# Kernel optimization log

Hardware: AMD Instinct MI355X
Metric: run time of the kernel (lower is better)

## Reference

```python
import jax, jax.numpy as jnp
import numpy as np

B = 4          # documents per batch
L = 128        # unique candidate entity links
S = 2048       # predicted spans (max over batch)
N = 1 + L + S  # root + links + spans


def setup_inputs() -> dict:
    key = jax.random.key(0)
    k1, k2, k3 = jax.random.split(key, 3)
    # coref/linking edge scores over [root | links | spans] x [root | links | spans]
    scores = jax.random.normal(k1, (B, N, N), dtype=jnp.float32) * 0.1
    eye = jnp.eye(N, dtype=jnp.float32)
    # z mask: all admissible edges -- no self loops, no incoming edges to root
    z_mask = jnp.ones((B, N, N), dtype=jnp.float32) * (1.0 - eye)[None]
    z_mask = z_mask.at[:, :, 0].set(0.0)
    # target mask: sparse subset of z edges + root->all so a spanning
    # arborescence always exists (mirrors the gold cluster / gold link edges)
    tgt = (jax.random.uniform(k2, (B, N, N)) < 0.05).astype(jnp.float32) * z_mask
    tgt = tgt.at[:, 0, 1:].set(1.0)
    # ragged valid lengths per batch element (1 + unique_links_len + n_pred_spans)
    lengths = jnp.array([N, N - 256, N - 512, N - 64], dtype=jnp.int32)
    return {"scores": scores, "target_mask": tgt, "z_mask": z_mask, "lengths": lengths}


def _mtt_log_partition(scores, mask, lengths):
    """Matrix-tree theorem log-partition: logdet of the root-minor of the
    Laplacian of exp(scores) restricted to edges in `mask` and to the first
    `lengths[b]` nodes of each batch element."""
    n = scores.shape[-1]
    valid = (jnp.arange(n)[None, :] < lengths[:, None]).astype(scores.dtype)  # [B,N]
    w = jnp.exp(scores) * mask * valid[:, :, None] * valid[:, None, :]        # [B,N,N]
    colsum = jnp.sum(w, axis=-2)                                              # incoming weight per node
    lap = colsum[:, :, None] * jnp.eye(n, dtype=scores.dtype)[None] - w       # L = D_in - W
    minor = lap[:, 1:, 1:]                                                    # drop root row/col
    # pad the diagonal of invalid (past-length) nodes with 1 so they
    # contribute logdet 0 instead of making the minor singular
    pad = 1.0 - valid[:, 1:]
    minor = minor + pad[:, :, None] * jnp.eye(n - 1, dtype=scores.dtype)[None]
    _, logdet = jnp.linalg.slogdet(minor)
    return logdet


def reference(scores, target_mask, z_mask, lengths):
    log_z = _mtt_log_partition(scores, z_mask, lengths)        # log partition over all arborescences
    log_t = _mtt_log_partition(scores, target_mask, lengths)   # log weight of gold arborescences
    return jnp.mean(log_z - log_t)                             # MTT negative log-likelihood
```

## Files before the change

### kernel.cpp

```cpp
#include <hip/hip_runtime.h>
#include <math.h>

#define NFULL 2177
#define NN    2176
#define NMAT  8
#define NBATCH 4
#define LDST  68
#define ATILES 68
#define FRAGM ((size_t)ATILES * 8 * 512)

typedef unsigned int  u32;
typedef unsigned short u16;
typedef __attribute__((ext_vector_type(8)))  short short8;
typedef __attribute__((ext_vector_type(16))) float f32x16;

__device__ inline void bf16split(float x, u16& hi, u16& lo) {
  u32 xb = __float_as_uint(x);
  u32 h = (xb + 0x7FFFu + ((xb >> 16) & 1u)) >> 16;
  float r = x - __uint_as_float(h << 16);
  u32 rb = __float_as_uint(r);
  u32 l = (rb + 0x7FFFu + ((rb >> 16) & 1u)) >> 16;
  hi = (u16)h; lo = (u16)l;
}

__device__ inline void packstore(short* P, size_t off, const u16 v[8]) {
  *(uint4*)(P + off) = make_uint4(v[0] | ((u32)v[1] << 16), v[2] | ((u32)v[3] << 16),
                                  v[4] | ((u32)v[5] << 16), v[6] | ((u32)v[7] << 16));
}

__device__ inline void frag_from_lds(const float* X, int locbase, int kl, int l,
                                     short* Phi, short* Plo, size_t off) {
  const float* p = &X[(locbase + (l & 31)) * LDST + kl];
  float4 v0 = *(const float4*)&p[0];
  float4 v1 = *(const float4*)&p[4];
  u16 hi[8], lo[8];
  bf16split(v0.x, hi[0], lo[0]); bf16split(v0.y, hi[1], lo[1]);
  bf16split(v0.z, hi[2], lo[2]); bf16split(v0.w, hi[3], lo[3]);
  bf16split(v1.x, hi[4], lo[4]); bf16split(v1.y, hi[5], lo[5]);
  bf16split(v1.z, hi[6], lo[6]); bf16split(v1.w, hi[7], lo[7]);
  packstore(Phi, off, hi);
  packstore(Plo, off, lo);
}

__device__ inline void load64(float* X, const float* A, int r0, int c0, int tid) {
#pragma unroll
  for (int it = 0; it < 4; ++it) {
    int f = tid + it * 256;
    int r = f >> 4, c4 = f & 15;
    *(float4*)&X[r * LDST + c4 * 4] = *(const float4*)&A[(size_t)(r0 + r) * NN + c0 + c4 * 4];
  }
}
__device__ inline void store64(const float* X, float* A, int r0, int c0, int tid) {
#pragma unroll
  for (int it = 0; it < 4; ++it) {
    int f = tid + it * 256;
    int r = f >> 4, c4 = f & 15;
    *(float4*)&A[(size_t)(r0 + r) * NN + c0 + c4 * 4] = *(const float4*)&X[r * LDST + c4 * 4];
  }
}

__device__ inline void factor64(float* D, int tid) {
  for (int j = 0; j < 63; ++j) {
    float inv = 1.0f / D[j * LDST + j];
    for (int r = j + 1 + tid; r < 64; r += 256) D[r * LDST + j] *= inv;
    __syncthreads();
    int cc = j + 1 + (tid & 63);
    for (int rr = j + 1 + (tid >> 6); rr < 64; rr += 4)
      if (cc < 64) D[rr * LDST + cc] -= D[rr * LDST + j] * D[j * LDST + cc];
    __syncthreads();
  }
}

__device__ inline void inv_upper64(const float* S, float* V, float* scr, int tid) {
  if (tid < 64) {
    int o = (tid >> 5) * 32, j = tid & 31;
    V[(o + j) * LDST + o + j] = 1.0f / S[(o + j) * LDST + o + j];
    for (int i = j - 1; i >= 0; --i) {
      float a = 0.f;
      for (int t = i + 1; t <= j; ++t) a += S[(o + i) * LDST + o + t] * V[(o + t) * LDST + o + j];
      V[(o + i) * LDST + o + j] = -a / S[(o + i) * LDST + o + i];
    }
    for (int i = j + 1; i < 32; ++i) V[(o + i) * LDST + o + j] = 0.f;
  }
  for (int e = tid; e < 1024; e += 256) V[(32 + (e >> 5)) * LDST + (e & 31)] = 0.f;
  __syncthreads();
  for (int e = tid; e < 1024; e += 256) {
    int a = e >> 5, c = e & 31; float s = 0.f;
    for (int t = 0; t < 32; ++t) s += S[a * LDST + 32 + t] * V[(32 + t) * LDST + 32 + c];
    scr[a * 33 + c] = s;
  }
  __syncthreads();
  for (int e = tid; e < 1024; e += 256) {
    int a = e >> 5, c = e & 31; float s = 0.f;
    for (int t = 0; t < 32; ++t) s += V[a * LDST + t] * scr[t * 33 + c];
    V[a * LDST + 32 + c] = -s;
  }
  __syncthreads();
}

__device__ inline void inv_lower64(const float* S, float* V, float* scr, int tid) {
  if (tid < 64) {
    int o = (tid >> 5) * 32, j = tid & 31;
    V[(o + j) * LDST + o + j] = 1.0f;
    for (int i = j + 1; i < 32; ++i) {
      float a = 0.f;
      for (int t = j; t < i; ++t) a += S[(o + i) * LDST + o + t] * V[(o + t) * LDST + o + j];
      V[(o + i) * LDST + o + j] = -a;
    }
    for (int i = 0; i < j; ++i) V[(o + i) * LDST + o + j] = 0.f;
  }
  for (int e = tid; e < 1024; e += 256) V[(e >> 5) * LDST + 32 + (e & 31)] = 0.f;
  __syncthreads();
  for (int e = tid; e < 1024; e += 256) {
    int a = e >> 5, c = e & 31; float s = 0.f;
    for (int t = 0; t < 32; ++t) s += S[(32 + a) * LDST + t] * V[t * LDST + c];
    scr[a * 33 + c] = s;
  }
  __syncthreads();
  for (int e = tid; e < 1024; e += 256) {
    int a = e >> 5, c = e & 31; float s = 0.f;
    for (int t = 0; t < 32; ++t) s += V[(32 + a) * LDST + 32 + t] * scr[t * 33 + c];
    V[(32 + a) * LDST + c] = -s;
  }
  __syncthreads();
}

__device__ inline void gemm64(const float* P, const float* Q, float acc[4][4], int r0, int c0) {
#pragma unroll
  for (int i = 0; i < 4; ++i)
#pragma unroll
    for (int j = 0; j < 4; ++j) acc[i][j] = 0.f;
  for (int kk = 0; kk < 64; kk += 4) {
    float4 p[4], q[4];
#pragma unroll
    for (int i = 0; i < 4; ++i) p[i] = *(const float4*)&P[(r0 + i) * LDST + kk];
#pragma unroll
    for (int t = 0; t < 4; ++t) q[t] = *(const float4*)&Q[(kk + t) * LDST + c0];
#pragma unroll
    for (int t = 0; t < 4; ++t) {
      float4 qt = q[t];
#pragma unroll
      for (int i = 0; i < 4; ++i) {
        float pv = ((const float*)&p[i])[t];
        acc[i][0] += pv * qt.x; acc[i][1] += pv * qt.y;
        acc[i][2] += pv * qt.z; acc[i][3] += pv * qt.w;
      }
    }
  }
}

__device__ inline void gemm64_bt(const float* P, const float* Q, float acc[4][4], int r0, int c0) {
#pragma unroll
  for (int i = 0; i < 4; ++i)
#pragma unroll
    for (int j = 0; j < 4; ++j) acc[i][j] = 0.f;
  for (int kk = 0; kk < 64; kk += 4) {
    float4 p[4], q[4];
#pragma unroll
    for (int i = 0; i < 4; ++i) p[i] = *(const float4*)&P[(r0 + i) * LDST + kk];
#pragma unroll
    for (int j = 0; j < 4; ++j) q[j] = *(const float4*)&Q[(c0 + j) * LDST + kk];
#pragma unroll
    for (int t = 0; t < 4; ++t)
#pragma unroll
      for (int i = 0; i < 4; ++i) {
        float pv = ((const float*)&p[i])[t];
#pragma unroll
        for (int j = 0; j < 4; ++j) acc[i][j] += pv * ((const float*)&q[j])[t];
      }
  }
}

__device__ inline void rmw_tile(float* __restrict__ A, int R0, int C0, const f32x16& ac) {
#pragma unroll
  for (int reg = 0; reg < 16; ++reg) {
    int row = R0 + (reg & 3) + 8 * (reg >> 2);
    A[(size_t)row * NN + C0] -= ac[reg];
  }
}


__global__ void init_cs_kernel(float* __restrict__ cs) {
  int i = blockIdx.x * blockDim.x + threadIdx.x;
  if (i < NMAT * NN) cs[i] = 0.f;
}

__global__ __launch_bounds__(256) void build_kernel(
    const float* __restrict__ scores, const float* __restrict__ zm,
    const float* __restrict__ tm, const int* __restrict__ lengths,
    float* __restrict__ M, float* __restrict__ cs) {
  int c = blockIdx.x * 256 + threadIdx.x;
  if (c >= NN) return;
  int b = blockIdx.z;
  int len = lengths[b];
  int j = c + 1;
  bool jv = (j < len);
  int r0 = blockIdx.y * 16;
  size_t sbase = (size_t)b * NFULL * NFULL;
  float* Mz = M + (size_t)b * NN * NN;
  float* Mt = M + (size_t)(NBATCH + b) * NN * NN;
  float az = 0.f, at = 0.f;
  for (int rr = 0; rr < 16; ++rr) {
    int r = r0 + rr, i = r + 1;
    float vz = 0.f, vt = 0.f;
    if (jv && i < len) {
      size_t off = sbase + (size_t)i * NFULL + j;
      float e = __expf(scores[off]);
      vz = e * zm[off];
      vt = e * tm[off];
    }
    Mz[(size_t)r * NN + c] = -vz;
    Mt[(size_t)r * NN + c] = -vt;
    az += vz; at += vt;
  }
  atomicAdd(&cs[b * NN + c], az);
  atomicAdd(&cs[(NBATCH + b) * NN + c], at);
}

__global__ void diag_fix_kernel(const float* __restrict__ scores,
                                const float* __restrict__ zm,
                                const float* __restrict__ tm,
                                const int* __restrict__ lengths,
                                const float* __restrict__ cs,
                                float* __restrict__ M) {
  int c = blockIdx.x * 256 + threadIdx.x;
  if (c >= NN) return;
  int m = blockIdx.y;
  int b = m & 3;
  const float* msk = (m < NBATCH) ? zm : tm;
  int len = lengths[b];
  int j = c + 1;
  float w0 = 0.f, pad = 1.f;
  if (j < len) {
    size_t off = (size_t)b * NFULL * NFULL + j;
    w0 = __expf(scores[off]) * msk[off];
    pad = 0.f;
  }
  M[(size_t)m * NN * NN + (size_t)c * NN + c] = cs[m * NN + c] + w0 + pad;
}


__device__ void psolve_body(float* __restrict__ M, short* __restrict__ Ahi,
                            short* __restrict__ Alo, int k0, int slab, int bx,
                            int m, int tid, float* X, float* Y, float* scr) {
  float* A = M + (size_t)m * NN * NN;
  int d0 = k0 + 64 * slab;
  int gr0 = k0 + 64 * (slab + 1) + bx * 64;
  load64(X, A, d0, d0, tid);
  __syncthreads();
  inv_upper64(X, Y, scr, tid);
  load64(X, A, gr0, d0, tid);
  __syncthreads();
  int r0 = (tid >> 4) * 4, c0 = (tid & 15) * 4;
  float acc[4][4];
  gemm64(X, Y, acc, r0, c0);
  __syncthreads();
#pragma unroll
  for (int i = 0; i < 4; ++i) {
    *(float4*)&A[(size_t)(gr0 + r0 + i) * NN + d0 + c0] =
        make_float4(acc[i][0], acc[i][1], acc[i][2], acc[i][3]);
    *(float4*)&X[(r0 + i) * LDST + c0] =
        make_float4(acc[i][0], acc[i][1], acc[i][2], acc[i][3]);
  }
  __syncthreads();
  size_t pbase = (size_t)m * FRAGM;
  for (int f = tid; f < 512; f += 256) {
    int l = f & 63, sl = (f >> 6) & 3, tt = (f >> 8) & 1;
    int tG = (gr0 >> 5) + tt, sG = slab * 4 + sl;
    int kl = sl * 16 + (l >> 5) * 8;
    size_t off = pbase + (((size_t)tG * 8 + sG) * 512 + (size_t)l * 8);
    frag_from_lds(X, tt * 32, kl, l, Ahi, Alo, off);
  }
}

__device__ void u12_body(float* __restrict__ M, short* __restrict__ Bhi,
                         short* __restrict__ Blo, int k0, int bx, int m, int tid,
                         float* X, float* Y, float* Z, float* scr) {
  float* A = M + (size_t)m * NN * NN;
  int cg0 = k0 + 128 + bx * 64;
  int r0 = (tid >> 4) * 4, c0 = (tid & 15) * 4;
  size_t pbase = (size_t)m * FRAGM;
  float acc[4][4];
  load64(X, A, k0, k0, tid);
  __syncthreads();
  inv_lower64(X, Y, scr, tid);
  load64(X, A, k0, cg0, tid);
  __syncthreads();
  gemm64(Y, X, acc, r0, c0);
  __syncthreads();
#pragma unroll
  for (int i = 0; i < 4; ++i)
#pragma unroll
    for (int j = 0; j < 4; ++j) Z[(c0 + j) * LDST + r0 + i] = acc[i][j];
  __syncthreads();
  for (int f = tid; f < 512; f += 256) {
    int l = f & 63, sl = (f >> 6) & 3, tt = (f >> 8) & 1;
    int tG = (cg0 >> 5) + tt;
    int kl = sl * 16 + (l >> 5) * 8;
    size_t off = pbase + (((size_t)tG * 8 + sl) * 512 + (size_t)l * 8);
    frag_from_lds(Z, tt * 32, kl, l, Bhi, Blo, off);
  }
  load64(X, A, k0 + 64, k0, tid);
  load64(Y, A, k0 + 64, cg0, tid);
  __syncthreads();
  gemm64_bt(X, Z, acc, r0, c0);
#pragma unroll
  for (int i = 0; i < 4; ++i)
#pragma unroll
    for (int j = 0; j < 4; ++j) {
      float v = Y[(r0 + i) * LDST + c0 + j] - acc[i][j];
      Y[(r0 + i) * LDST + c0 + j] = v;
    }
  __syncthreads();
  load64(X, A, k0 + 64, k0 + 64, tid);
  __syncthreads();
  inv_lower64(X, Z, scr, tid);
  gemm64(Z, Y, acc, r0, c0);
  __syncthreads();
#pragma unroll
  for (int i = 0; i < 4; ++i)
#pragma unroll
    for (int j = 0; j < 4; ++j) X[(c0 + j) * LDST + r0 + i] = acc[i][j];
  __syncthreads();
  for (int f = tid; f < 512; f += 256) {
    int l = f & 63, sl = (f >> 6) & 3, tt = (f >> 8) & 1;
    int tG = (cg0 >> 5) + tt;
    int kl = sl * 16 + (l >> 5) * 8;
    size_t off = pbase + (((size_t)tG * 8 + 4 + sl) * 512 + (size_t)l * 8);
    frag_from_lds(X, tt * 32, kl, l, Bhi, Blo, off);
  }
}

__global__ __launch_bounds__(256) void ps0_kernel(float* __restrict__ M,
    short* __restrict__ Ahi, short* __restrict__ Alo, int k0) {
  __shared__ float lds[2 * 64 * LDST + 32 * 33];
  psolve_body(M, Ahi, Alo, k0, 0, blockIdx.x, blockIdx.y, threadIdx.x,
              lds, lds + 64 * LDST, lds + 2 * 64 * LDST);
}

__global__ __launch_bounds__(256) void step_mid(float* __restrict__ M,
    short* __restrict__ Ahi, short* __restrict__ Alo,
    short* __restrict__ Bhi, short* __restrict__ Blo, int k0) {
  __shared__ float lds[3 * 64 * LDST + 32 * 33];
  if (blockIdx.z == 0)
    psolve_body(M, Ahi, Alo, k0, 1, blockIdx.x, blockIdx.y, threadIdx.x,
                lds, lds + 64 * LDST, lds + 3 * 64 * LDST);
  else
    u12_body(M, Bhi, Blo, k0, blockIdx.x, blockIdx.y, threadIdx.x,
             lds, lds + 64 * LDST, lds + 2 * 64 * LDST, lds + 3 * 64 * LDST);
}

__global__ __launch_bounds__(256) void fd_first(float* __restrict__ M,
    short* __restrict__ ibhi, short* __restrict__ iblo) {
  __shared__ float lds[2 * 64 * LDST + 32 * 33];
  float* X = lds; float* Y = lds + 64 * LDST; float* scr = lds + 2 * 64 * LDST;
  int m = blockIdx.x, tid = threadIdx.x;
  float* A = M + (size_t)m * NN * NN;
  load64(X, A, 0, 0, tid);
  __syncthreads();
  factor64(X, tid);
  store64(X, A, 0, 0, tid);
  inv_lower64(X, Y, scr, tid);
  load64(X, A, 0, 64, tid);
  __syncthreads();
  float acc[4][4]; int r0 = (tid >> 4) * 4, c0 = (tid & 15) * 4;
  gemm64(Y, X, acc, r0, c0);
  __syncthreads();
#pragma unroll
  for (int i = 0; i < 4; ++i)
#pragma unroll
    for (int j = 0; j < 4; ++j) X[(c0 + j) * LDST + r0 + i] = acc[i][j];
  __syncthreads();
  for (int f = tid; f < 512; f += 256) {
    int l = f & 63, sl = (f >> 6) & 3, tt = (f >> 8) & 1;
    int kl = sl * 16 + (l >> 5) * 8;
    size_t off = (((size_t)m * 2 + tt) * 4 + sl) * 512 + (size_t)l * 8;
    frag_from_lds(X, tt * 32, kl, l, ibhi, iblo, off);
  }
}

__global__ __launch_bounds__(256) void ig_kernel(float* __restrict__ M,
    const short* __restrict__ Ahi, const short* __restrict__ Alo,
    const short* __restrict__ ibhi, const short* __restrict__ iblo, int k0) {
  __shared__ float X[64 * LDST];
  int m = blockIdx.y, tid = threadIdx.x;
  float* A = M + (size_t)m * NN * NN;
  int w = tid >> 6, l = tid & 63;
  int nr0 = (NN - k0 - 64) / 64;
  int T = blockIdx.x * 4 + w;
  if (T < nr0) {
    int gr0 = k0 + 64 + T * 64;
    size_t pbase = (size_t)m * FRAGM;
    int tA = gr0 >> 5;
    f32x16 acc[2][2];
#pragma unroll
    for (int i = 0; i < 2; ++i)
#pragma unroll
      for (int j = 0; j < 2; ++j)
#pragma unroll
        for (int q = 0; q < 16; ++q) acc[i][j][q] = 0.f;
#pragma unroll
    for (int s = 0; s < 4; ++s) {
      short8 ah[2], al[2], bh[2], bl[2];
#pragma unroll
      for (int t = 0; t < 2; ++t) {
        size_t oa = pbase + (((size_t)(tA + t) * 8 + s) * 512 + (size_t)l * 8);
        ah[t] = *(const short8*)(Ahi + oa);
        al[t] = *(const short8*)(Alo + oa);
        size_t ob = (((size_t)m * 2 + t) * 4 + s) * 512 + (size_t)l * 8;
        bh[t] = *(const short8*)(ibhi + ob);
        bl[t] = *(const short8*)(iblo + ob);
      }
#pragma unroll
      for (int i = 0; i < 2; ++i)
#pragma unroll
        for (int j = 0; j < 2; ++j) {
          acc[i][j] = __builtin_amdgcn_mfma_f32_32x32x16_bf16(ah[i], bh[j], acc[i][j], 0, 0, 0);
          acc[i][j] = __builtin_amdgcn_mfma_f32_32x32x16_bf16(ah[i], bl[j], acc[i][j], 0, 0, 0);
          acc[i][j] = __builtin_amdgcn_mfma_f32_32x32x16_bf16(al[i], bh[j], acc[i][j], 0, 0, 0);
        }
    }
    int lr = 4 * (l >> 5), lc = l & 31;
#pragma unroll
    for (int i = 0; i < 2; ++i)
#pragma unroll
      for (int j = 0; j < 2; ++j)
        rmw_tile(A, gr0 + i * 32 + lr, k0 + 64 + j * 32 + lc, acc[i][j]);
  }
  if (blockIdx.x == 0) {
    __syncthreads();
    load64(X, A, k0 + 64, k0 + 64, tid);
    __syncthreads();
    factor64(X, tid);
    store64(X, A, k0 + 64, k0 + 64, tid);
  }
}

__global__ __launch_bounds__(256) void gemm2_kernel(float* __restrict__ M,
    const short* __restrict__ Ahi, const short* __restrict__ Alo,
    const short* __restrict__ Bhi, const short* __restrict__ Blo,
    short* __restrict__ ibhi, short* __restrict__ iblo, int k0) {
  __shared__ float lds[2 * 64 * LDST + 32 * 33];
  float* X = lds; float* Y = lds + 64 * LDST; float* scr = lds + 2 * 64 * LDST;
  int m = blockIdx.z, tid = threadIdx.x;
  float* A = M + (size_t)m * NN * NN;
  size_t pbase = (size_t)m * FRAGM;
  int w = tid >> 6, l = tid & 63, wr = w >> 1, wc = w & 1;
  int base = k0 + 128;
  int tb = base >> 5;
  int tr = tb + blockIdx.y * 4 + wr * 2;
  int tc = tb + blockIdx.x * 4 + wc * 2;
  f32x16 acc[2][2];
#pragma unroll
  for (int i = 0; i < 2; ++i)
#pragma unroll
    for (int j = 0; j < 2; ++j)
#pragma unroll
      for (int q = 0; q < 16; ++q) acc[i][j][q] = 0.f;
#pragma unroll
  for (int s = 0; s < 8; ++s) {
    short8 ah[2], al[2], bh[2], bl[2];
#pragma unroll
    for (int t = 0; t < 2; ++t) {
      size_t oa = pbase + (((size_t)(tr + t) * 8 + s) * 512 + (size_t)l * 8);
      ah[t] = *(const short8*)(Ahi + oa);
      al[t] = *(const short8*)(Alo + oa);
      size_t ob = pbase + (((size_t)(tc + t) * 8 + s) * 512 + (size_t)l * 8);
      bh[t] = *(const short8*)(Bhi + ob);
      bl[t] = *(const short8*)(Blo + ob);
    }
#pragma unroll
    for (int i = 0; i < 2; ++i)
#pragma unroll
      for (int j = 0; j < 2; ++j) {
        acc[i][j] = __builtin_amdgcn_mfma_f32_32x32x16_bf16(ah[i], bh[j], acc[i][j], 0, 0, 0);
        acc[i][j] = __builtin_amdgcn_mfma_f32_32x32x16_bf16(ah[i], bl[j], acc[i][j], 0, 0, 0);
        acc[i][j] = __builtin_amdgcn_mfma_f32_32x32x16_bf16(al[i], bh[j], acc[i][j], 0, 0, 0);
      }
  }
  int lr = 4 * (l >> 5), lc = l & 31;
#pragma unroll
  for (int i = 0; i < 2; ++i)
#pragma unroll
    for (int j = 0; j < 2; ++j)
      rmw_tile(A, (tr + i) * 32 + lr, (tc + j) * 32 + lc, acc[i][j]);
  if (blockIdx.x == 0 && blockIdx.y == 0) {
    __syncthreads();
    load64(X, A, base, base, tid);
    __syncthreads();
    factor64(X, tid);
    store64(X, A, base, base, tid);
    inv_lower64(X, Y, scr, tid);
    load64(X, A, base, base + 64, tid);
    __syncthreads();
    float a4[4][4]; int r0 = (tid >> 4) * 4, c0 = (tid & 15) * 4;
    gemm64(Y, X, a4, r0, c0);
    __syncthreads();
#pragma unroll
    for (int i = 0; i < 4; ++i)
#pragma unroll
      for (int j = 0; j < 4; ++j) X[(c0 + j) * LDST + r0 + i] = a4[i][j];
    __syncthreads();
    for (int f = tid; f < 512; f += 256) {
      int ll = f & 63, sl = (f >> 6) & 3, tt = (f >> 8) & 1;
      int kl = sl * 16 + (ll >> 5) * 8;
      size_t off = (((size_t)m * 2 + tt) * 4 + sl) * 512 + (size_t)ll * 8;
      frag_from_lds(X, tt * 32, kl, ll, ibhi, iblo, off);
    }
  }
}


__global__ void logdet_kernel(const float* __restrict__ Mb, double* __restrict__ dlog) {
  int m = blockIdx.x;
  const float* A = Mb + (size_t)m * NN * NN;
  double s = 0.0;
  for (int i = threadIdx.x; i < NN; i += 256)
    s += (double)logf(fabsf(A[(size_t)i * NN + i]));
  __shared__ double red[256];
  red[threadIdx.x] = s;
  __syncthreads();
  for (int k = 128; k > 0; k >>= 1) {
    if (threadIdx.x < k) red[threadIdx.x] += red[threadIdx.x + k];
    __syncthreads();
  }
  if (threadIdx.x == 0) dlog[m] = red[0];
}

__global__ void final_kernel(const double* __restrict__ dlog, float* __restrict__ out) {
  if (threadIdx.x == 0) {
    double acc = 0.0;
    for (int b = 0; b < NBATCH; ++b) acc += dlog[b] - dlog[NBATCH + b];
    out[0] = (float)(acc * 0.25);
  }
}


extern "C" void kernel_launch(void* const* d_in, const int* in_sizes, int n_in,
                              void* d_out, int out_size, void* d_ws, size_t ws_size,
                              hipStream_t stream) {
  const float* scores  = (const float*)d_in[0];
  const float* tm      = (const float*)d_in[1];
  const float* zm      = (const float*)d_in[2];
  const int*   lengths = (const int*)d_in[3];
  float* out = (float*)d_out;

  char* p = (char*)d_ws;
  float* M = (float*)p;      p += (size_t)NMAT * NN * NN * sizeof(float);
  short* Ahi = (short*)p;    p += NMAT * FRAGM * sizeof(short);
  short* Alo = (short*)p;    p += NMAT * FRAGM * sizeof(short);
  short* Bhi = (short*)p;    p += NMAT * FRAGM * sizeof(short);
  short* Blo = (short*)p;    p += NMAT * FRAGM * sizeof(short);
  short* ibhi = (short*)p;   p += (size_t)NMAT * 2 * 4 * 512 * sizeof(short);
  short* iblo = (short*)p;   p += (size_t)NMAT * 2 * 4 * 512 * sizeof(short);
  float* cs = (float*)p;     p += (size_t)NMAT * NN * sizeof(float);
  double* dlog = (double*)p;

  init_cs_kernel<<<(NMAT * NN + 255) / 256, 256, 0, stream>>>(cs);
  build_kernel<<<dim3((NN + 255) / 256, NN / 16, NBATCH), 256, 0, stream>>>(
      scores, zm, tm, lengths, M, cs);
  diag_fix_kernel<<<dim3((NN + 255) / 256, NMAT), 256, 0, stream>>>(
      scores, zm, tm, lengths, cs, M);
  fd_first<<<NMAT, 256, 0, stream>>>(M, ibhi, iblo);

  for (int k0 = 0; k0 < NN - 64; k0 += 128) {
    int rem2 = NN - k0 - 128;
    int nr0 = (NN - k0 - 64) / 64;
    ps0_kernel<<<dim3(nr0, NMAT), 256, 0, stream>>>(M, Ahi, Alo, k0);
    ig_kernel<<<dim3((nr0 + 3) / 4, NMAT), 256, 0, stream>>>(M, Ahi, Alo, ibhi, iblo, k0);
    if (rem2 > 0) {
      step_mid<<<dim3(rem2 / 64, NMAT, 2), 256, 0, stream>>>(M, Ahi, Alo, Bhi, Blo, k0);
      gemm2_kernel<<<dim3(rem2 / 128, rem2 / 128, NMAT), 256, 0, stream>>>(
          M, Ahi, Alo, Bhi, Blo, ibhi, iblo, k0);
    }
  }

  logdet_kernel<<<NMAT, 256, 0, stream>>>(M, dlog);
  final_kernel<<<1, 64, 0, stream>>>(dlog, out);
}
```

Baseline: 5.127 ms.

## Replace per-step LU kernel launches with one persistent cooperative kernel using grid barriers

The blocked LU factorization is now a single persistent kernel of 512 blocks that loops over all panel steps and uses a spin-wait global barrier in place of several kernel launches per step. The small 64x64 triangular solves are moved onto bf16-split MFMA. The diagonal-block factor and its log-determinant are computed inside the loop and accumulated atomically, so the separate logdet and final kernels are gone. This removes launch overhead across roughly 17 steps times 4 kernels. It risks deadlock if all 512 blocks cannot be resident at once, since it depends on occupancy of 2 blocks per CU, and it adds global-barrier cost plus serialized corner work.

```diff
diff --git a/kernel.cpp b/kernel.cpp
--- a/kernel.cpp
+++ b/kernel.cpp
@@ -6,41 +6,75 @@
 #define NMAT  8
 #define NBATCH 4
 #define LDST  68
-#define ATILES 68
-#define FRAGM ((size_t)ATILES * 8 * 512)
-
-typedef unsigned int  u32;
+#define FRAGM ((size_t)68 * 8 * 512)
+#define GRIDB 512
+
+typedef unsigned int   u32;
 typedef unsigned short u16;
 typedef __attribute__((ext_vector_type(8)))  short short8;
 typedef __attribute__((ext_vector_type(16))) float f32x16;
+
 
 __device__ inline void bf16split(float x, u16& hi, u16& lo) {
   u32 xb = __float_as_uint(x);
   u32 h = (xb + 0x7FFFu + ((xb >> 16) & 1u)) >> 16;
   float r = x - __uint_as_float(h << 16);
   u32 rb = __float_as_uint(r);
-  u32 l = (rb + 0x7FFFu + ((rb >> 16) & 1u)) >> 16;
-  hi = (u16)h; lo = (u16)l;
-}
-
+  u32 l2 = (rb + 0x7FFFu + ((rb >> 16) & 1u)) >> 16;
+  hi = (u16)h; lo = (u16)l2;
+}
 __device__ inline void packstore(short* P, size_t off, const u16 v[8]) {
   *(uint4*)(P + off) = make_uint4(v[0] | ((u32)v[1] << 16), v[2] | ((u32)v[3] << 16),
                                   v[4] | ((u32)v[5] << 16), v[6] | ((u32)v[7] << 16));
 }
-
-__device__ inline void frag_from_lds(const float* X, int locbase, int kl, int l,
-                                     short* Phi, short* Plo, size_t off) {
-  const float* p = &X[(locbase + (l & 31)) * LDST + kl];
-  float4 v0 = *(const float4*)&p[0];
-  float4 v1 = *(const float4*)&p[4];
+__device__ inline f32x16 zero16() {
+  f32x16 z;
+#pragma unroll
+  for (int i = 0; i < 16; ++i) z[i] = 0.f;
+  return z;
+}
+__device__ inline f32x16 mfma3(short8 ah, short8 al, short8 bh, short8 bl, f32x16 c) {
+  c = __builtin_amdgcn_mfma_f32_32x32x16_bf16(ah, bh, c, 0, 0, 0);
+  c = __builtin_amdgcn_mfma_f32_32x32x16_bf16(ah, bl, c, 0, 0, 0);
+  c = __builtin_amdgcn_mfma_f32_32x32x16_bf16(al, bh, c, 0, 0, 0);
+  return c;
+}
+__device__ inline void split8(const float v[8], short8& h, short8& l) {
+  u16 hh, ll;
+#pragma unroll
+  for (int j = 0; j < 8; ++j) { bf16split(v[j], hh, ll); h[j] = (short)hh; l[j] = (short)ll; }
+}
+__device__ inline void aop_lds(const float* X, int row, int kl, short8& h, short8& l) {
+  const float* p = &X[row * LDST + kl];
+  float4 a = *(const float4*)p, b = *(const float4*)(p + 4);
+  float v[8] = {a.x, a.y, a.z, a.w, b.x, b.y, b.z, b.w};
+  split8(v, h, l);
+}
+__device__ inline void bop_lds(const float* X, int col, int kl, short8& h, short8& l) {
+  float v[8];
+#pragma unroll
+  for (int j = 0; j < 8; ++j) v[j] = X[(kl + j) * LDST + col];
+  split8(v, h, l);
+}
+__device__ inline void pack_row(const float* X, int rowbase, int kl, int l,
+                                short* Phi, short* Plo, size_t off) {
+  const float* p = &X[(rowbase + (l & 31)) * LDST + kl];
+  float4 a = *(const float4*)p, b = *(const float4*)(p + 4);
+  float v[8] = {a.x, a.y, a.z, a.w, b.x, b.y, b.z, b.w};
   u16 hi[8], lo[8];
-  bf16split(v0.x, hi[0], lo[0]); bf16split(v0.y, hi[1], lo[1]);
-  bf16split(v0.z, hi[2], lo[2]); bf16split(v0.w, hi[3], lo[3]);
-  bf16split(v1.x, hi[4], lo[4]); bf16split(v1.y, hi[5], lo[5]);
-  bf16split(v1.z, hi[6], lo[6]); bf16split(v1.w, hi[7], lo[7]);
-  packstore(Phi, off, hi);
-  packstore(Plo, off, lo);
-}
+#pragma unroll
+  for (int j = 0; j < 8; ++j) bf16split(v[j], hi[j], lo[j]);
+  packstore(Phi, off, hi); packstore(Plo, off, lo);
+}
+__device__ inline void pack_col(const float* X, int colbase, int kl, int l,
+                                short* Phi, short* Plo, size_t off) {
+  int col = colbase + (l & 31);
+  u16 hi[8], lo[8];
+#pragma unroll
+  for (int j = 0; j < 8; ++j) bf16split(X[(kl + j) * LDST + col], hi[j], lo[j]);
+  packstore(Phi, off, hi); packstore(Plo, off, lo);
+}
+
 
 __device__ inline void load64(float* X, const float* A, int r0, int c0, int tid) {
 #pragma unroll
@@ -48,14 +82,6 @@
     int f = tid + it * 256;
     int r = f >> 4, c4 = f & 15;
     *(float4*)&X[r * LDST + c4 * 4] = *(const float4*)&A[(size_t)(r0 + r) * NN + c0 + c4 * 4];
-  }
-}
-__device__ inline void store64(const float* X, float* A, int r0, int c0, int tid) {
-#pragma unroll
-  for (int it = 0; it < 4; ++it) {
-    int f = tid + it * 256;
-    int r = f >> 4, c4 = f & 15;
-    *(float4*)&A[(size_t)(r0 + r) * NN + c0 + c4 * 4] = *(const float4*)&X[r * LDST + c4 * 4];
   }
 }
 
@@ -125,52 +151,26 @@
   __syncthreads();
 }
 
-__device__ inline void gemm64(const float* P, const float* Q, float acc[4][4], int r0, int c0) {
-#pragma unroll
-  for (int i = 0; i < 4; ++i)
-#pragma unroll
-    for (int j = 0; j < 4; ++j) acc[i][j] = 0.f;
-  for (int kk = 0; kk < 64; kk += 4) {
-    float4 p[4], q[4];
-#pragma unroll
-    for (int i = 0; i < 4; ++i) p[i] = *(const float4*)&P[(r0 + i) * LDST + kk];
-#pragma unroll
-    for (int t = 0; t < 4; ++t) q[t] = *(const float4*)&Q[(kk + t) * LDST + c0];
-#pragma unroll
-    for (int t = 0; t < 4; ++t) {
-      float4 qt = q[t];
-#pragma unroll
-      for (int i = 0; i < 4; ++i) {
-        float pv = ((const float*)&p[i])[t];
-        acc[i][0] += pv * qt.x; acc[i][1] += pv * qt.y;
-        acc[i][2] += pv * qt.z; acc[i][3] += pv * qt.w;
-      }
-    }
-  }
-}
-
-__device__ inline void gemm64_bt(const float* P, const float* Q, float acc[4][4], int r0, int c0) {
-#pragma unroll
-  for (int i = 0; i < 4; ++i)
-#pragma unroll
-    for (int j = 0; j < 4; ++j) acc[i][j] = 0.f;
-  for (int kk = 0; kk < 64; kk += 4) {
-    float4 p[4], q[4];
-#pragma unroll
-    for (int i = 0; i < 4; ++i) p[i] = *(const float4*)&P[(r0 + i) * LDST + kk];
-#pragma unroll
-    for (int j = 0; j < 4; ++j) q[j] = *(const float4*)&Q[(c0 + j) * LDST + kk];
-#pragma unroll
-    for (int t = 0; t < 4; ++t)
-#pragma unroll
-      for (int i = 0; i < 4; ++i) {
-        float pv = ((const float*)&p[i])[t];
-#pragma unroll
-        for (int j = 0; j < 4; ++j) acc[i][j] += pv * ((const float*)&q[j])[t];
-      }
-  }
-}
-
+__device__ inline void logdet64(const float* X, double* dst, int tid, float* scr) {
+  __syncthreads();
+  if (tid < 64) scr[tid] = logf(fabsf(X[tid * LDST + tid]));
+  __syncthreads();
+  if (tid == 0) {
+    double s = 0.0;
+    for (int i = 0; i < 64; ++i) s += (double)scr[i];
+    atomicAdd(dst, s);
+  }
+  __syncthreads();
+}
+
+__device__ inline void acc_to_lds(float* Y, int rt, int ct, int l, const f32x16& a) {
+  int lr = 4 * (l >> 5), lc = l & 31;
+#pragma unroll
+  for (int reg = 0; reg < 16; ++reg) {
+    int ro = lr + (reg & 3) + 8 * (reg >> 2);
+    Y[(rt * 32 + ro) * LDST + ct * 32 + lc] = a[reg];
+  }
+}
 __device__ inline void rmw_tile(float* __restrict__ A, int R0, int C0, const f32x16& ac) {
 #pragma unroll
   for (int reg = 0; reg < 16; ++reg) {
@@ -178,11 +178,74 @@
     A[(size_t)row * NN + C0] -= ac[reg];
   }
 }
-
-
-__global__ void init_cs_kernel(float* __restrict__ cs) {
+__device__ inline void dstage(const float* A, int gR, int gC, int lR, int lC,
+                              const f32x16& a, float* X, int lr, int lc) {
+#pragma unroll
+  for (int reg = 0; reg < 16; ++reg) {
+    int ro = lr + (reg & 3) + 8 * (reg >> 2);
+    X[(lR + ro) * LDST + lC + lc] = A[(size_t)(gR + ro) * NN + gC + lc] - a[reg];
+  }
+}
+
+__device__ inline void packA64(const float* Y, short* Phi, short* Plo,
+                               size_t pb, int tG0, int s0, int tid) {
+  for (int f = tid; f < 512; f += 256) {
+    int l = f & 63, sl = (f >> 6) & 3, tt = (f >> 8) & 1;
+    int kl = sl * 16 + (l >> 5) * 8;
+    size_t off = pb + (((size_t)(tG0 + tt) * 8 + s0 + sl) * 512 + (size_t)l * 8);
+    pack_row(Y, tt * 32, kl, l, Phi, Plo, off);
+  }
+}
+__device__ inline void packB64(const float* Y, short* Phi, short* Plo,
+                               size_t pb, int tG0, int s0, int tid) {
+  for (int f = tid; f < 512; f += 256) {
+    int l = f & 63, sl = (f >> 6) & 3, tt = (f >> 8) & 1;
+    int kl = sl * 16 + (l >> 5) * 8;
+    size_t off = pb + (((size_t)(tG0 + tt) * 8 + s0 + sl) * 512 + (size_t)l * 8);
+    pack_col(Y, tt * 32, kl, l, Phi, Plo, off);
+  }
+}
+__device__ inline size_t ivoff(int m, int slot, int tt, int s, int l) {
+  return (((size_t)(m * 2 + slot) * 2 + tt) * 4 + s) * 512 + (size_t)l * 8;
+}
+__device__ inline void packInvB(const float* Y, short* Phi, short* Plo, int m, int slot, int tid) {
+  for (int f = tid; f < 512; f += 256) {
+    int l = f & 63, sl = (f >> 6) & 3, tt = (f >> 8) & 1;
+    int kl = sl * 16 + (l >> 5) * 8;
+    pack_col(Y, tt * 32, kl, l, Phi, Plo, ivoff(m, slot, tt, sl, l));
+  }
+}
+__device__ inline void packInvA(const float* Y, short* Phi, short* Plo, int m, int slot, int tid) {
+  for (int f = tid; f < 512; f += 256) {
+    int l = f & 63, sl = (f >> 6) & 3, tt = (f >> 8) & 1;
+    int kl = sl * 16 + (l >> 5) * 8;
+    pack_row(Y, tt * 32, kl, l, Phi, Plo, ivoff(m, slot, tt, sl, l));
+  }
+}
+
+__device__ inline void gsync(u32* bar, u32* gen) {
+  __syncthreads();
+  if (threadIdx.x == 0) {
+    __threadfence();
+    u32 g = ++(*gen);
+    atomicAdd(bar, 1u);
+    u32 target = g * (u32)GRIDB;
+    long long guard = 0;
+    while (__hip_atomic_load(bar, __ATOMIC_RELAXED, __HIP_MEMORY_SCOPE_AGENT) < target) {
+      if (++guard > 1000000000LL) break;
+    }
+    __threadfence();
+  }
+  __syncthreads();
+}
+
+
+__global__ void init_kernel(float* __restrict__ cs, double* __restrict__ dlog,
+                            u32* __restrict__ bar) {
   int i = blockIdx.x * blockDim.x + threadIdx.x;
   if (i < NMAT * NN) cs[i] = 0.f;
+  if (i < NMAT) dlog[i] = 0.0;
+  if (i == 0) bar[0] = 0u;
 }
 
 __global__ __launch_bounds__(256) void build_kernel(
@@ -240,298 +303,258 @@
 }
 
 
-__device__ void psolve_body(float* __restrict__ M, short* __restrict__ Ahi,
-                            short* __restrict__ Alo, int k0, int slab, int bx,
-                            int m, int tid, float* X, float* Y, float* scr) {
-  float* A = M + (size_t)m * NN * NN;
-  int d0 = k0 + 64 * slab;
-  int gr0 = k0 + 64 * (slab + 1) + bx * 64;
-  load64(X, A, d0, d0, tid);
-  __syncthreads();
-  inv_upper64(X, Y, scr, tid);
-  load64(X, A, gr0, d0, tid);
-  __syncthreads();
-  int r0 = (tid >> 4) * 4, c0 = (tid & 15) * 4;
-  float acc[4][4];
-  gemm64(X, Y, acc, r0, c0);
-  __syncthreads();
-#pragma unroll
-  for (int i = 0; i < 4; ++i) {
-    *(float4*)&A[(size_t)(gr0 + r0 + i) * NN + d0 + c0] =
-        make_float4(acc[i][0], acc[i][1], acc[i][2], acc[i][3]);
-    *(float4*)&X[(r0 + i) * LDST + c0] =
-        make_float4(acc[i][0], acc[i][1], acc[i][2], acc[i][3]);
-  }
-  __syncthreads();
-  size_t pbase = (size_t)m * FRAGM;
-  for (int f = tid; f < 512; f += 256) {
-    int l = f & 63, sl = (f >> 6) & 3, tt = (f >> 8) & 1;
-    int tG = (gr0 >> 5) + tt, sG = slab * 4 + sl;
-    int kl = sl * 16 + (l >> 5) * 8;
-    size_t off = pbase + (((size_t)tG * 8 + sG) * 512 + (size_t)l * 8);
-    frag_from_lds(X, tt * 32, kl, l, Ahi, Alo, off);
-  }
-}
-
-__device__ void u12_body(float* __restrict__ M, short* __restrict__ Bhi,
-                         short* __restrict__ Blo, int k0, int bx, int m, int tid,
-                         float* X, float* Y, float* Z, float* scr) {
-  float* A = M + (size_t)m * NN * NN;
-  int cg0 = k0 + 128 + bx * 64;
-  int r0 = (tid >> 4) * 4, c0 = (tid & 15) * 4;
-  size_t pbase = (size_t)m * FRAGM;
-  float acc[4][4];
-  load64(X, A, k0, k0, tid);
-  __syncthreads();
-  inv_lower64(X, Y, scr, tid);
-  load64(X, A, k0, cg0, tid);
-  __syncthreads();
-  gemm64(Y, X, acc, r0, c0);
-  __syncthreads();
-#pragma unroll
-  for (int i = 0; i < 4; ++i)
-#pragma unroll
-    for (int j = 0; j < 4; ++j) Z[(c0 + j) * LDST + r0 + i] = acc[i][j];
-  __syncthreads();
-  for (int f = tid; f < 512; f += 256) {
-    int l = f & 63, sl = (f >> 6) & 3, tt = (f >> 8) & 1;
-    int tG = (cg0 >> 5) + tt;
-    int kl = sl * 16 + (l >> 5) * 8;
-    size_t off = pbase + (((size_t)tG * 8 + sl) * 512 + (size_t)l * 8);
-    frag_from_lds(Z, tt * 32, kl, l, Bhi, Blo, off);
-  }
-  load64(X, A, k0 + 64, k0, tid);
-  load64(Y, A, k0 + 64, cg0, tid);
-  __syncthreads();
-  gemm64_bt(X, Z, acc, r0, c0);
-#pragma unroll
-  for (int i = 0; i < 4; ++i)
-#pragma unroll
-    for (int j = 0; j < 4; ++j) {
-      float v = Y[(r0 + i) * LDST + c0 + j] - acc[i][j];
-      Y[(r0 + i) * LDST + c0 + j] = v;
-    }
-  __syncthreads();
-  load64(X, A, k0 + 64, k0 + 64, tid);
-  __syncthreads();
-  inv_lower64(X, Z, scr, tid);
-  gemm64(Z, Y, acc, r0, c0);
-  __syncthreads();
-#pragma unroll
-  for (int i = 0; i < 4; ++i)
-#pragma unroll
-    for (int j = 0; j < 4; ++j) X[(c0 + j) * LDST + r0 + i] = acc[i][j];
-  __syncthreads();
-  for (int f = tid; f < 512; f += 256) {
-    int l = f & 63, sl = (f >> 6) & 3, tt = (f >> 8) & 1;
-    int tG = (cg0 >> 5) + tt;
-    int kl = sl * 16 + (l >> 5) * 8;
-    size_t off = pbase + (((size_t)tG * 8 + 4 + sl) * 512 + (size_t)l * 8);
-    frag_from_lds(X, tt * 32, kl, l, Bhi, Blo, off);
-  }
-}
-
-__global__ __launch_bounds__(256) void ps0_kernel(float* __restrict__ M,
-    short* __restrict__ Ahi, short* __restrict__ Alo, int k0) {
-  __shared__ float lds[2 * 64 * LDST + 32 * 33];
-  psolve_body(M, Ahi, Alo, k0, 0, blockIdx.x, blockIdx.y, threadIdx.x,
-              lds, lds + 64 * LDST, lds + 2 * 64 * LDST);
-}
-
-__global__ __launch_bounds__(256) void step_mid(float* __restrict__ M,
+__global__ __launch_bounds__(256, 2) void lu_coop(
+    float* __restrict__ M,
     short* __restrict__ Ahi, short* __restrict__ Alo,
-    short* __restrict__ Bhi, short* __restrict__ Blo, int k0) {
-  __shared__ float lds[3 * 64 * LDST + 32 * 33];
-  if (blockIdx.z == 0)
-    psolve_body(M, Ahi, Alo, k0, 1, blockIdx.x, blockIdx.y, threadIdx.x,
-                lds, lds + 64 * LDST, lds + 3 * 64 * LDST);
-  else
-    u12_body(M, Bhi, Blo, k0, blockIdx.x, blockIdx.y, threadIdx.x,
-             lds, lds + 64 * LDST, lds + 2 * 64 * LDST, lds + 3 * 64 * LDST);
-}
-
-__global__ __launch_bounds__(256) void fd_first(float* __restrict__ M,
-    short* __restrict__ ibhi, short* __restrict__ iblo) {
-  __shared__ float lds[2 * 64 * LDST + 32 * 33];
-  float* X = lds; float* Y = lds + 64 * LDST; float* scr = lds + 2 * 64 * LDST;
-  int m = blockIdx.x, tid = threadIdx.x;
-  float* A = M + (size_t)m * NN * NN;
-  load64(X, A, 0, 0, tid);
-  __syncthreads();
-  factor64(X, tid);
-  store64(X, A, 0, 0, tid);
-  inv_lower64(X, Y, scr, tid);
-  load64(X, A, 0, 64, tid);
-  __syncthreads();
-  float acc[4][4]; int r0 = (tid >> 4) * 4, c0 = (tid & 15) * 4;
-  gemm64(Y, X, acc, r0, c0);
-  __syncthreads();
-#pragma unroll
-  for (int i = 0; i < 4; ++i)
-#pragma unroll
-    for (int j = 0; j < 4; ++j) X[(c0 + j) * LDST + r0 + i] = acc[i][j];
-  __syncthreads();
-  for (int f = tid; f < 512; f += 256) {
-    int l = f & 63, sl = (f >> 6) & 3, tt = (f >> 8) & 1;
-    int kl = sl * 16 + (l >> 5) * 8;
-    size_t off = (((size_t)m * 2 + tt) * 4 + sl) * 512 + (size_t)l * 8;
-    frag_from_lds(X, tt * 32, kl, l, ibhi, iblo, off);
-  }
-}
-
-__global__ __launch_bounds__(256) void ig_kernel(float* __restrict__ M,
-    const short* __restrict__ Ahi, const short* __restrict__ Alo,
-    const short* __restrict__ ibhi, const short* __restrict__ iblo, int k0) {
+    short* __restrict__ Bhi, short* __restrict__ Blo,
+    short* __restrict__ IAhi, short* __restrict__ IAlo,
+    short* __restrict__ IBhi, short* __restrict__ IBlo,
+    double* __restrict__ dlog, float* __restrict__ out, u32* __restrict__ bar) {
   __shared__ float X[64 * LDST];
-  int m = blockIdx.y, tid = threadIdx.x;
-  float* A = M + (size_t)m * NN * NN;
+  __shared__ float Y[64 * LDST];
+  __shared__ float scr[32 * 33];
+  __shared__ u32 gen_s;
+  int tid = threadIdx.x;
+  if (tid == 0) gen_s = 0u;
+  int nb = GRIDB, bid = blockIdx.x;
   int w = tid >> 6, l = tid & 63;
-  int nr0 = (NN - k0 - 64) / 64;
-  int T = blockIdx.x * 4 + w;
-  if (T < nr0) {
-    int gr0 = k0 + 64 + T * 64;
-    size_t pbase = (size_t)m * FRAGM;
-    int tA = gr0 >> 5;
-    f32x16 acc[2][2];
-#pragma unroll
-    for (int i = 0; i < 2; ++i)
-#pragma unroll
-      for (int j = 0; j < 2; ++j)
-#pragma unroll
-        for (int q = 0; q < 16; ++q) acc[i][j][q] = 0.f;
-#pragma unroll
-    for (int s = 0; s < 4; ++s) {
-      short8 ah[2], al[2], bh[2], bl[2];
-#pragma unroll
-      for (int t = 0; t < 2; ++t) {
-        size_t oa = pbase + (((size_t)(tA + t) * 8 + s) * 512 + (size_t)l * 8);
-        ah[t] = *(const short8*)(Ahi + oa);
-        al[t] = *(const short8*)(Alo + oa);
-        size_t ob = (((size_t)m * 2 + t) * 4 + s) * 512 + (size_t)l * 8;
-        bh[t] = *(const short8*)(ibhi + ob);
-        bl[t] = *(const short8*)(iblo + ob);
-      }
-#pragma unroll
-      for (int i = 0; i < 2; ++i)
-#pragma unroll
-        for (int j = 0; j < 2; ++j) {
-          acc[i][j] = __builtin_amdgcn_mfma_f32_32x32x16_bf16(ah[i], bh[j], acc[i][j], 0, 0, 0);
-          acc[i][j] = __builtin_amdgcn_mfma_f32_32x32x16_bf16(ah[i], bl[j], acc[i][j], 0, 0, 0);
-          acc[i][j] = __builtin_amdgcn_mfma_f32_32x32x16_bf16(al[i], bh[j], acc[i][j], 0, 0, 0);
-        }
-    }
-    int lr = 4 * (l >> 5), lc = l & 31;
-#pragma unroll
-    for (int i = 0; i < 2; ++i)
-#pragma unroll
-      for (int j = 0; j < 2; ++j)
-        rmw_tile(A, gr0 + i * 32 + lr, k0 + 64 + j * 32 + lc, acc[i][j]);
-  }
-  if (blockIdx.x == 0) {
-    __syncthreads();
-    load64(X, A, k0 + 64, k0 + 64, tid);
+  int lr = 4 * (l >> 5), lc = l & 31;
+
+  for (int m = bid; m < NMAT; m += nb) {
+    float* A = M + (size_t)m * NN * NN;
+    load64(X, A, 0, 0, tid);
     __syncthreads();
     factor64(X, tid);
-    store64(X, A, k0 + 64, k0 + 64, tid);
-  }
-}
-
-__global__ __launch_bounds__(256) void gemm2_kernel(float* __restrict__ M,
-    const short* __restrict__ Ahi, const short* __restrict__ Alo,
-    const short* __restrict__ Bhi, const short* __restrict__ Blo,
-    short* __restrict__ ibhi, short* __restrict__ iblo, int k0) {
-  __shared__ float lds[2 * 64 * LDST + 32 * 33];
-  float* X = lds; float* Y = lds + 64 * LDST; float* scr = lds + 2 * 64 * LDST;
-  int m = blockIdx.z, tid = threadIdx.x;
-  float* A = M + (size_t)m * NN * NN;
-  size_t pbase = (size_t)m * FRAGM;
-  int w = tid >> 6, l = tid & 63, wr = w >> 1, wc = w & 1;
-  int base = k0 + 128;
-  int tb = base >> 5;
-  int tr = tb + blockIdx.y * 4 + wr * 2;
-  int tc = tb + blockIdx.x * 4 + wc * 2;
-  f32x16 acc[2][2];
-#pragma unroll
-  for (int i = 0; i < 2; ++i)
-#pragma unroll
-    for (int j = 0; j < 2; ++j)
-#pragma unroll
-      for (int q = 0; q < 16; ++q) acc[i][j][q] = 0.f;
-#pragma unroll
-  for (int s = 0; s < 8; ++s) {
-    short8 ah[2], al[2], bh[2], bl[2];
-#pragma unroll
-    for (int t = 0; t < 2; ++t) {
-      size_t oa = pbase + (((size_t)(tr + t) * 8 + s) * 512 + (size_t)l * 8);
-      ah[t] = *(const short8*)(Ahi + oa);
-      al[t] = *(const short8*)(Alo + oa);
-      size_t ob = pbase + (((size_t)(tc + t) * 8 + s) * 512 + (size_t)l * 8);
-      bh[t] = *(const short8*)(Bhi + ob);
-      bl[t] = *(const short8*)(Blo + ob);
-    }
-#pragma unroll
-    for (int i = 0; i < 2; ++i)
-#pragma unroll
-      for (int j = 0; j < 2; ++j) {
-        acc[i][j] = __builtin_amdgcn_mfma_f32_32x32x16_bf16(ah[i], bh[j], acc[i][j], 0, 0, 0);
-        acc[i][j] = __builtin_amdgcn_mfma_f32_32x32x16_bf16(ah[i], bl[j], acc[i][j], 0, 0, 0);
-        acc[i][j] = __builtin_amdgcn_mfma_f32_32x32x16_bf16(al[i], bh[j], acc[i][j], 0, 0, 0);
+    logdet64(X, &dlog[m], tid, scr);
+    inv_upper64(X, Y, scr, tid);
+    packInvB(Y, IBhi, IBlo, m, 0, tid);
+    __syncthreads();
+    inv_lower64(X, Y, scr, tid);
+    packInvA(Y, IAhi, IAlo, m, 0, tid);
+    __syncthreads();
+  }
+  gsync(bar, &gen_s);
+
+  for (int k0 = 0; k0 < NN - 64; k0 += 128) {
+    int rem  = NN - k0 - 64;
+    int rem2 = NN - k0 - 128;
+    int nch  = rem / 64;
+    int rt = w >> 1, ct = w & 1;
+
+    {
+      int njob = 2 * nch * NMAT;
+      for (int job = bid; job < njob; job += nb) {
+        int m = job % NMAT, jt = job / NMAT;
+        float* A = M + (size_t)m * NN * NN;
+        size_t pb = (size_t)m * FRAGM;
+        if (jt < nch) {
+          int r0 = k0 + 64 + 64 * jt;
+          load64(X, A, r0, k0, tid);
+          __syncthreads();
+          f32x16 acc = zero16();
+#pragma unroll
+          for (int s = 0; s < 4; ++s) {
+            short8 ah, al, bh, bl;
+            aop_lds(X, rt * 32 + lc, s * 16 + (l >> 5) * 8, ah, al);
+            size_t io = ivoff(m, 0, ct, s, l);
+            bh = *(const short8*)(IBhi + io); bl = *(const short8*)(IBlo + io);
+            acc = mfma3(ah, al, bh, bl, acc);
+          }
+          __syncthreads();
+          acc_to_lds(Y, rt, ct, l, acc);
+          __syncthreads();
+          packA64(Y, Ahi, Alo, pb, r0 >> 5, 0, tid);
+          __syncthreads();
+        } else {
+          int c0 = k0 + 64 + 64 * (jt - nch);
+          load64(X, A, k0, c0, tid);
+          __syncthreads();
+          f32x16 acc = zero16();
+#pragma unroll
+          for (int s = 0; s < 4; ++s) {
+            short8 ah, al, bh, bl;
+            size_t io = ivoff(m, 0, rt, s, l);
+            ah = *(const short8*)(IAhi + io); al = *(const short8*)(IAlo + io);
+            bop_lds(X, ct * 32 + lc, s * 16 + (l >> 5) * 8, bh, bl);
+            acc = mfma3(ah, al, bh, bl, acc);
+          }
+          __syncthreads();
+          acc_to_lds(Y, rt, ct, l, acc);
+          __syncthreads();
+          packB64(Y, Bhi, Blo, pb, c0 >> 5, 0, tid);
+          __syncthreads();
+        }
       }
-  }
-  int lr = 4 * (l >> 5), lc = l & 31;
-#pragma unroll
-  for (int i = 0; i < 2; ++i)
-#pragma unroll
-    for (int j = 0; j < 2; ++j)
-      rmw_tile(A, (tr + i) * 32 + lr, (tc + j) * 32 + lc, acc[i][j]);
-  if (blockIdx.x == 0 && blockIdx.y == 0) {
-    __syncthreads();
-    load64(X, A, base, base, tid);
-    __syncthreads();
-    factor64(X, tid);
-    store64(X, A, base, base, tid);
-    inv_lower64(X, Y, scr, tid);
-    load64(X, A, base, base + 64, tid);
-    __syncthreads();
-    float a4[4][4]; int r0 = (tid >> 4) * 4, c0 = (tid & 15) * 4;
-    gemm64(Y, X, a4, r0, c0);
-    __syncthreads();
-#pragma unroll
-    for (int i = 0; i < 4; ++i)
-#pragma unroll
-      for (int j = 0; j < 4; ++j) X[(c0 + j) * LDST + r0 + i] = a4[i][j];
-    __syncthreads();
-    for (int f = tid; f < 512; f += 256) {
-      int ll = f & 63, sl = (f >> 6) & 3, tt = (f >> 8) & 1;
-      int kl = sl * 16 + (ll >> 5) * 8;
-      size_t off = (((size_t)m * 2 + tt) * 4 + sl) * 512 + (size_t)ll * 8;
-      frag_from_lds(X, tt * 32, kl, ll, ibhi, iblo, off);
-    }
-  }
-}
-
-
-__global__ void logdet_kernel(const float* __restrict__ Mb, double* __restrict__ dlog) {
-  int m = blockIdx.x;
-  const float* A = Mb + (size_t)m * NN * NN;
-  double s = 0.0;
-  for (int i = threadIdx.x; i < NN; i += 256)
-    s += (double)logf(fabsf(A[(size_t)i * NN + i]));
-  __shared__ double red[256];
-  red[threadIdx.x] = s;
-  __syncthreads();
-  for (int k = 128; k > 0; k >>= 1) {
-    if (threadIdx.x < k) red[threadIdx.x] += red[threadIdx.x + k];
-    __syncthreads();
-  }
-  if (threadIdx.x == 0) dlog[m] = red[0];
-}
-
-__global__ void final_kernel(const double* __restrict__ dlog, float* __restrict__ out) {
-  if (threadIdx.x == 0) {
-    double acc = 0.0;
-    for (int b = 0; b < NBATCH; ++b) acc += dlog[b] - dlog[NBATCH + b];
-    out[0] = (float)(acc * 0.25);
+    }
+    gsync(bar, &gen_s);
+
+    {
+      int njob = nch * NMAT;
+      int tb = (k0 + 64) >> 5;
+      for (int job = bid; job < njob; job += nb) {
+        int m = job % NMAT, j = job / NMAT;
+        float* A = M + (size_t)m * NN * NN;
+        size_t pb = (size_t)m * FRAGM;
+        int r0 = k0 + 64 + 64 * j;
+        f32x16 acc = zero16();
+#pragma unroll
+        for (int s = 0; s < 4; ++s) {
+          size_t oa = pb + (((size_t)((r0 >> 5) + rt) * 8 + s) * 512 + (size_t)l * 8);
+          size_t ob = pb + (((size_t)(tb + ct) * 8 + s) * 512 + (size_t)l * 8);
+          short8 ah = *(const short8*)(Ahi + oa), al = *(const short8*)(Alo + oa);
+          short8 bh = *(const short8*)(Bhi + ob), bl = *(const short8*)(Blo + ob);
+          acc = mfma3(ah, al, bh, bl, acc);
+        }
+        if (j > 0) {
+          rmw_tile(A, r0 + rt * 32 + lr, k0 + 64 + ct * 32 + lc, acc);
+        } else {
+          dstage(A, r0 + rt * 32, k0 + 64 + ct * 32, rt * 32, ct * 32, acc, X, lr, lc);
+          __syncthreads();
+          factor64(X, tid);
+          logdet64(X, &dlog[m], tid, scr);
+          inv_upper64(X, Y, scr, tid);
+          packInvB(Y, IBhi, IBlo, m, 1, tid);
+          __syncthreads();
+          inv_lower64(X, Y, scr, tid);
+          packInvA(Y, IAhi, IAlo, m, 1, tid);
+          __syncthreads();
+        }
+      }
+    }
+    gsync(bar, &gen_s);
+
+    if (rem2 > 0) {
+      {
+        int nch2 = rem2 / 64;
+        int njob = 2 * nch2 * NMAT;
+        int tl1 = (k0 + 64) >> 5;
+        for (int job = bid; job < njob; job += nb) {
+          int m = job % NMAT, jt = job / NMAT;
+          float* A = M + (size_t)m * NN * NN;
+          size_t pb = (size_t)m * FRAGM;
+          if (jt < nch2) {
+            int r0 = k0 + 128 + 64 * jt;
+            load64(X, A, r0, k0 + 64, tid);
+            __syncthreads();
+            f32x16 acc = zero16();
+#pragma unroll
+            for (int s = 0; s < 4; ++s) {
+              short8 ah, al, bh, bl;
+              aop_lds(X, rt * 32 + lc, s * 16 + (l >> 5) * 8, ah, al);
+              size_t io = ivoff(m, 1, ct, s, l);
+              bh = *(const short8*)(IBhi + io); bl = *(const short8*)(IBlo + io);
+              acc = mfma3(ah, al, bh, bl, acc);
+            }
+            __syncthreads();
+            acc_to_lds(Y, rt, ct, l, acc);
+            __syncthreads();
+            packA64(Y, Ahi, Alo, pb, r0 >> 5, 4, tid);
+            __syncthreads();
+          } else {
+            int c0 = k0 + 128 + 64 * (jt - nch2);
+            f32x16 acc = zero16();
+#pragma unroll
+            for (int s = 0; s < 4; ++s) {
+              size_t oa = pb + (((size_t)(tl1 + rt) * 8 + s) * 512 + (size_t)l * 8);
+              size_t ob = pb + (((size_t)((c0 >> 5) + ct) * 8 + s) * 512 + (size_t)l * 8);
+              short8 ah = *(const short8*)(Ahi + oa), al = *(const short8*)(Alo + oa);
+              short8 bh = *(const short8*)(Bhi + ob), bl = *(const short8*)(Blo + ob);
+              acc = mfma3(ah, al, bh, bl, acc);
+            }
+            load64(X, A, k0 + 64, c0, tid);
+            __syncthreads();
+#pragma unroll
+            for (int reg = 0; reg < 16; ++reg) {
+              int ro = lr + (reg & 3) + 8 * (reg >> 2);
+              X[(rt * 32 + ro) * LDST + ct * 32 + lc] -= acc[reg];
+            }
+            __syncthreads();
+            f32x16 a2 = zero16();
+#pragma unroll
+            for (int s = 0; s < 4; ++s) {
+              short8 ah, al, bh, bl;
+              size_t io = ivoff(m, 1, rt, s, l);
+              ah = *(const short8*)(IAhi + io); al = *(const short8*)(IAlo + io);
+              bop_lds(X, ct * 32 + lc, s * 16 + (l >> 5) * 8, bh, bl);
+              a2 = mfma3(ah, al, bh, bl, a2);
+            }
+            __syncthreads();
+            acc_to_lds(Y, rt, ct, l, a2);
+            __syncthreads();
+            packB64(Y, Bhi, Blo, pb, c0 >> 5, 4, tid);
+            __syncthreads();
+          }
+        }
+      }
+      gsync(bar, &gen_s);
+
+      {
+        int nt = rem2 / 128;
+        int njob = nt * nt * NMAT;
+        int tbase = (k0 + 128) >> 5;
+        for (int job = bid; job < njob; job += nb) {
+          int m = job % NMAT, t = job / NMAT;
+          int by = t / nt, bx = t % nt;
+          float* A = M + (size_t)m * NN * NN;
+          size_t pb = (size_t)m * FRAGM;
+          int wr = w >> 1, wc = w & 1;
+          int tr = tbase + by * 4 + wr * 2;
+          int tc = tbase + bx * 4 + wc * 2;
+          f32x16 acc[2][2];
+          acc[0][0] = zero16(); acc[0][1] = zero16();
+          acc[1][0] = zero16(); acc[1][1] = zero16();
+#pragma unroll
+          for (int s = 0; s < 8; ++s) {
+            short8 ah[2], al[2], bh[2], bl[2];
+#pragma unroll
+            for (int t2 = 0; t2 < 2; ++t2) {
+              size_t oa = pb + (((size_t)(tr + t2) * 8 + s) * 512 + (size_t)l * 8);
+              ah[t2] = *(const short8*)(Ahi + oa); al[t2] = *(const short8*)(Alo + oa);
+              size_t ob = pb + (((size_t)(tc + t2) * 8 + s) * 512 + (size_t)l * 8);
+              bh[t2] = *(const short8*)(Bhi + ob); bl[t2] = *(const short8*)(Blo + ob);
+            }
+#pragma unroll
+            for (int i = 0; i < 2; ++i)
+#pragma unroll
+              for (int j2 = 0; j2 < 2; ++j2)
+                acc[i][j2] = mfma3(ah[i], al[i], bh[j2], bl[j2], acc[i][j2]);
+          }
+          bool corner = (bx == 0 && by == 0);
+          if (!corner || w != 0) {
+#pragma unroll
+            for (int i = 0; i < 2; ++i)
+#pragma unroll
+              for (int j2 = 0; j2 < 2; ++j2)
+                rmw_tile(A, (tr + i) * 32 + lr, (tc + j2) * 32 + lc, acc[i][j2]);
+          } else {
+#pragma unroll
+            for (int i = 0; i < 2; ++i)
+#pragma unroll
+              for (int j2 = 0; j2 < 2; ++j2)
+                dstage(A, (tr + i) * 32, (tc + j2) * 32, i * 32, j2 * 32, acc[i][j2], X, lr, lc);
+          }
+          if (corner) {
+            __syncthreads();
+            factor64(X, tid);
+            logdet64(X, &dlog[m], tid, scr);
+            inv_upper64(X, Y, scr, tid);
+            packInvB(Y, IBhi, IBlo, m, 0, tid);
+            __syncthreads();
+            inv_lower64(X, Y, scr, tid);
+            packInvA(Y, IAhi, IAlo, m, 0, tid);
+            __syncthreads();
+          }
+        }
+      }
+      gsync(bar, &gen_s);
+    }
+  }
+
+  gsync(bar, &gen_s);
+  if (bid == 0 && tid == 0) {
+    double s = 0.0;
+    for (int b = 0; b < NBATCH; ++b) s += dlog[b] - dlog[NBATCH + b];
+    out[0] = (float)(s * 0.25);
   }
 }
 
@@ -551,30 +574,20 @@
   short* Alo = (short*)p;    p += NMAT * FRAGM * sizeof(short);
   short* Bhi = (short*)p;    p += NMAT * FRAGM * sizeof(short);
   short* Blo = (short*)p;    p += NMAT * FRAGM * sizeof(short);
-  short* ibhi = (short*)p;   p += (size_t)NMAT * 2 * 4 * 512 * sizeof(short);
-  short* iblo = (short*)p;   p += (size_t)NMAT * 2 * 4 * 512 * sizeof(short);
+  size_t ivsz = (size_t)NMAT * 2 * 2 * 4 * 512;
+  short* IAhi = (short*)p;   p += ivsz * sizeof(short);
+  short* IAlo = (short*)p;   p += ivsz * sizeof(short);
+  short* IBhi = (short*)p;   p += ivsz * sizeof(short);
+  short* IBlo = (short*)p;   p += ivsz * sizeof(short);
   float* cs = (float*)p;     p += (size_t)NMAT * NN * sizeof(float);
-  double* dlog = (double*)p;
-
-  init_cs_kernel<<<(NMAT * NN + 255) / 256, 256, 0, stream>>>(cs);
+  double* dlog = (double*)p; p += (size_t)NMAT * sizeof(double);
+  u32* bar = (u32*)p;
+
+  init_kernel<<<(NMAT * NN + 255) / 256, 256, 0, stream>>>(cs, dlog, bar);
   build_kernel<<<dim3((NN + 255) / 256, NN / 16, NBATCH), 256, 0, stream>>>(
       scores, zm, tm, lengths, M, cs);
   diag_fix_kernel<<<dim3((NN + 255) / 256, NMAT), 256, 0, stream>>>(
       scores, zm, tm, lengths, cs, M);
-  fd_first<<<NMAT, 256, 0, stream>>>(M, ibhi, iblo);
-
-  for (int k0 = 0; k0 < NN - 64; k0 += 128) {
-    int rem2 = NN - k0 - 128;
-    int nr0 = (NN - k0 - 64) / 64;
-    ps0_kernel<<<dim3(nr0, NMAT), 256, 0, stream>>>(M, Ahi, Alo, k0);
-    ig_kernel<<<dim3((nr0 + 3) / 4, NMAT), 256, 0, stream>>>(M, Ahi, Alo, ibhi, iblo, k0);
-    if (rem2 > 0) {
-      step_mid<<<dim3(rem2 / 64, NMAT, 2), 256, 0, stream>>>(M, Ahi, Alo, Bhi, Blo, k0);
-      gemm2_kernel<<<dim3(rem2 / 128, rem2 / 128, NMAT), 256, 0, stream>>>(
-          M, Ahi, Alo, Bhi, Blo, ibhi, iblo, k0);
-    }
-  }
-
-  logdet_kernel<<<NMAT, 256, 0, stream>>>(M, dlog);
-  final_kernel<<<1, 64, 0, stream>>>(dlog, out);
-}
+  lu_coop<<<GRIDB, 256, 0, stream>>>(M, Ahi, Alo, Bhi, Blo,
+                                     IAhi, IAlo, IBhi, IBlo, dlog, out, bar);
+}
```

Result: slower. 7.466 ms (+45.6%).
